# Kernel tuning notes

Measured on AMD Instinct MI355X. Metric: run time of the kernel, lower is better.

The kernel has to match this reference:

```python
import jax, jax.numpy as jnp
import numpy as np

# Dimensions
B, T, H = 4, 4096, 2048          # batch, seq, hidden
NH = 16                           # total hash heads = (max_ngram-1)*n_head_per_ngram
PER_HEAD_VOCAB = 100000
DH = 64                           # per-head embedding dim
E = NH * DH                       # engram_hidden_size = 1024
G = 4                             # hc_mult
K = 4                             # kernel_size
DIL = 3                           # dilation = max_ngram_size
EPS_RMS = 1.1920929e-07           # torch RMSNorm default eps (fp32 finfo eps)
EPS_SC = 1e-5                     # ShortConv RMSNorm eps


def setup_inputs() -> dict:
    key = jax.random.key(0)
    ks = jax.random.split(key, 12)
    hidden_states = jax.random.normal(ks[0], (T, B, H), dtype=jnp.float32)
    hash_ids = jax.random.randint(ks[1], (B, T, NH), 0, PER_HEAD_VOCAB)
    emb_table = jax.random.normal(ks[2], (NH * PER_HEAD_VOCAB, DH), dtype=jnp.float32)
    s = 0.02
    key_W = jax.random.normal(ks[3], (G, H, E), dtype=jnp.float32) * s
    key_b = jax.random.normal(ks[4], (G, H), dtype=jnp.float32) * s
    value_W = jax.random.normal(ks[5], (H, E), dtype=jnp.float32) * s
    value_b = jax.random.normal(ks[6], (H,), dtype=jnp.float32) * s
    norm1_w = jnp.ones((G, H), dtype=jnp.float32)
    norm2_w = jnp.ones((G, H), dtype=jnp.float32)
    sc_norm_w = jnp.ones((G, H), dtype=jnp.float32)
    conv_w = jax.random.normal(ks[7], (G * H, K), dtype=jnp.float32) * 0.1
    return {"hidden_states": hidden_states, "hash_ids": hash_ids, "emb_table": emb_table,
            "key_W": key_W, "key_b": key_b, "value_W": value_W, "value_b": value_b,
            "norm1_w": norm1_w, "norm2_w": norm2_w, "sc_norm_w": sc_norm_w, "conv_w": conv_w}


def _rms(x, eps):
    return x * jax.lax.rsqrt(jnp.mean(x * x, axis=-1, keepdims=True) + eps)


def reference(hidden_states, hash_ids, emb_table, key_W, key_b, value_W, value_b,
              norm1_w, norm2_w, sc_norm_w, conv_w):
    # --- precompute_embeddings: hashed multi-head gather ---
    offsets = jnp.arange(NH, dtype=hash_ids.dtype) * PER_HEAD_VOCAB
    emb = emb_table[hash_ids + offsets]              # [B,T,NH,DH]
    emb = emb.reshape(B, T, E)                       # [B,T,E]

    # --- forward ---
    hs = jnp.transpose(hidden_states, (1, 0, 2))     # [B,T,H]
    # per-group key projection + RMSNorm (vectorized over G)
    keys = jnp.einsum('bte,ghe->btgh', emb, key_W) + key_b   # [B,T,G,H]
    nk = _rms(keys, EPS_RMS) * norm1_w               # [B,T,G,H]
    nq = _rms(hs, EPS_RMS)[:, :, None, :] * norm2_w  # [B,T,G,H]
    gate = jnp.sum(nk * nq, axis=-1) / np.sqrt(H)    # [B,T,G]
    gate = jnp.sqrt(jnp.maximum(jnp.abs(gate), 1e-6)) * jnp.sign(gate)
    gate = jax.nn.sigmoid(gate)[..., None]           # [B,T,G,1]
    value = gate * (emb @ value_W.T + value_b)[:, :, None, :]   # [B,T,G,H]

    # --- ShortConv: per-group RMSNorm -> causal dilated depthwise conv -> SiLU ---
    xn = _rms(value, EPS_SC) * sc_norm_w             # [B,T,G,H]
    x_bct = xn.reshape(B, T, G * H).transpose(0, 2, 1)  # [B,G*H,T]
    y = jax.lax.conv_general_dilated(
        x_bct, conv_w[:, None, :],                   # rhs [C,1,K]
        window_strides=(1,), padding=[((K - 1) * DIL, 0)],
        rhs_dilation=(DIL,), dimension_numbers=('NCH', 'OIH', 'NCH'),
        feature_group_count=G * H)                   # [B,G*H,T]
    y = jax.nn.silu(y)
    y = y.transpose(0, 2, 1).reshape(B, T, G, H)

    out = (value + y).mean(axis=2)                   # [B,T,H]
    return jnp.transpose(out, (1, 0, 2))             # [S,B,H]
```

## Files before the change

kernel.cpp:

```cpp
#include <hip/hip_runtime.h>
#include <hip/hip_bf16.h>

#define BB 4
#define TT 4096
#define HH 2048
#define NHH 16
#define VOC 100000
#define EE 1024
#define GG 4
#define BT (BB*TT)
#define NKEY (GG*HH)
#define NTOT (NKEY+HH)
#define NPART 32
#define TCV 48

static constexpr float EPS_RMS = 1.1920929e-07f;
static constexpr float EPS_SC  = 1e-5f;
static constexpr float INV_SQRT_H = 0.02209708691207961f;

using f32x4 = __attribute__((ext_vector_type(4))) float;
using f32x2 = __attribute__((ext_vector_type(2))) float;
using s8v   = __attribute__((ext_vector_type(8))) short;
using gvoid = __attribute__((address_space(1))) const void;
using lvoid = __attribute__((address_space(3))) void;

__device__ __forceinline__ unsigned short f2bf(float f){
  union { __hip_bfloat16 h; unsigned short u; } cv;
  cv.h = __float2bfloat16(f);
  return cv.u;
}
__device__ __forceinline__ float bf2f(unsigned short u){
  union { float f; unsigned u; } cv;
  cv.u = ((unsigned)u) << 16;
  return cv.f;
}

__global__ __launch_bounds__(256) void convw_kern(const float* __restrict__ kW,
    const float* __restrict__ vW, unsigned short* __restrict__ Wc){
  const long idx  = (long)blockIdx.x*256 + threadIdx.x;
  const long base = idx*4;
  const long KN   = (long)NKEY*EE;
  float4 v;
  if (base < KN) v = *(const float4*)(kW + base);
  else           v = *(const float4*)(vW + (base - KN));
  ushort4 o; o.x=f2bf(v.x); o.y=f2bf(v.y); o.z=f2bf(v.z); o.w=f2bf(v.w);
  *(ushort4*)(Wc + base) = o;
}

__global__ __launch_bounds__(256) void prep_kern(const int* __restrict__ hids,
    const float* __restrict__ table, unsigned short* __restrict__ emb,
    const float* __restrict__ hs, float* __restrict__ rq,
    unsigned short* __restrict__ hsbf){
  const int p = blockIdx.x, tid = threadIdx.x;
  const int e = tid*4, head = e>>6, d = e&63;
  const long row = (long)hids[p*NHH + head] + (long)head*VOC;
  const float4 v = *(const float4*)(table + row*64 + d);
  ushort4 o; o.x=f2bf(v.x); o.y=f2bf(v.y); o.z=f2bf(v.z); o.w=f2bf(v.w);
  *(ushort4*)(emb + (size_t)p*EE + e) = o;
  const int b = p>>12, t = p&4095;
  const float* hrow = hs + ((size_t)t*BB + b)*HH;
  const int e8 = tid*8;
  float4 v0 = *(const float4*)(hrow+e8);
  float4 v1 = *(const float4*)(hrow+e8+4);
  ushort4 hb0; hb0.x=f2bf(v0.x); hb0.y=f2bf(v0.y); hb0.z=f2bf(v0.z); hb0.w=f2bf(v0.w);
  ushort4 hb1; hb1.x=f2bf(v1.x); hb1.y=f2bf(v1.y); hb1.z=f2bf(v1.z); hb1.w=f2bf(v1.w);
  *(ushort4*)(hsbf + (size_t)p*HH + e8)     = hb0;
  *(ushort4*)(hsbf + (size_t)p*HH + e8 + 4) = hb1;
  float s = v0.x*v0.x+v0.y*v0.y+v0.z*v0.z+v0.w*v0.w
          + v1.x*v1.x+v1.y*v1.y+v1.z*v1.z+v1.w*v1.w;
  #pragma unroll
  for (int of=32;of>=1;of>>=1) s += __shfl_xor(s,of);
  __shared__ float red[4];
  if ((tid&63)==0) red[tid>>6] = s;
  __syncthreads();
  if (tid==0){
    float tot = red[0]+red[1]+red[2]+red[3];
    rq[p] = rsqrtf(tot*(1.0f/HH) + EPS_RMS);
  }
}

__global__ __launch_bounds__(512, 2) void gemm8(
    const unsigned short* __restrict__ A, const unsigned short* __restrict__ Bw,
    const float* __restrict__ key_b, const float* __restrict__ value_b,
    const float* __restrict__ n1w, const float* __restrict__ n2w,
    const unsigned short* __restrict__ hsbf, unsigned short* __restrict__ vlinb,
    f32x2* __restrict__ sdp, float* __restrict__ vsqp)
{
  __shared__ unsigned short sh[65536];
  const int tid = threadIdx.x, w = tid>>6, l = tid&63;
  const int wm = w>>2, wn = w&3;
  const int lg = l&15, lr = l>>4;
  const int wg  = blockIdx.x;
  const int swz = (wg&7)*320 + (wg>>3);
  const int tM  = swz/40, tN = swz - tM*40;
  const int Mrow0 = tM*256, Nrow0 = tN*256;

  const int lp = l>>3, lcs = (l&7)^lp;
  const size_t aoffT = (size_t)(Mrow0 + w*16 + lp)*EE + lcs*8;
  const size_t boffT = (size_t)(Nrow0 + w*16 + lp)*EE + lcs*8;
  const int c0 = lr ^ (lg&7);
  const unsigned aBase = (unsigned)(wm*8192 + lg*64);
  const unsigned bBase = (unsigned)(16384 + (wn>>1)*8192 + (wn&1)*4096 + lg*64);

  f32x4 acc[8][4] = {};
  s8v aR0[4], aR1[4], bR0[4], bR1[4];

#define STAGEH(ISB, H, KT, SB) { \
    const unsigned short* s0_ = ((ISB) ? (Bw + boffT) : (A + aoffT)) + (H)*131072 + (KT)*64; \
    const unsigned d0_ = (SB)*32768 + (ISB)*16384 + (H)*8192 + w*1024; \
    __builtin_amdgcn_global_load_lds((gvoid*)s0_,        (lvoid*)(sh + d0_),       16, 0, 0); \
    __builtin_amdgcn_global_load_lds((gvoid*)(s0_+8192), (lvoid*)(sh + d0_ + 512), 16, 0, 0); \
  }
#define STAGE4(KT, SB) { STAGEH(0,0,KT,SB); STAGEH(0,1,KT,SB); STAGEH(1,0,KT,SB); STAGEH(1,1,KT,SB); }

#define BAR() { asm volatile("" ::: "memory"); __builtin_amdgcn_s_barrier(); asm volatile("" ::: "memory"); }

#define RD_A(CB, KK, MH, DST) { \
    const unsigned short* p_ = sh + (CB)*32768 + aBase; \
    const unsigned ck_ = (unsigned)((c0 ^ ((KK)<<2))<<3); \
    DST[0] = *(const s8v*)(p_ + ((MH)*4+0)*1024 + ck_); \
    DST[1] = *(const s8v*)(p_ + ((MH)*4+1)*1024 + ck_); \
    DST[2] = *(const s8v*)(p_ + ((MH)*4+2)*1024 + ck_); \
    DST[3] = *(const s8v*)(p_ + ((MH)*4+3)*1024 + ck_); }

#define RD_B(CB, KK, DST) { \
    const unsigned short* p_ = sh + (CB)*32768 + bBase; \
    const unsigned ck_ = (unsigned)((c0 ^ ((KK)<<2))<<3); \
    DST[0] = *(const s8v*)(p_ + 0*1024 + ck_); \
    DST[1] = *(const s8v*)(p_ + 1*1024 + ck_); \
    DST[2] = *(const s8v*)(p_ + 2*1024 + ck_); \
    DST[3] = *(const s8v*)(p_ + 3*1024 + ck_); }

#define MM(MH, AF, BF) { \
    __builtin_amdgcn_s_setprio(1); \
    _Pragma("unroll") \
    for (int mf=0; mf<4; mf++) \
      _Pragma("unroll") \
      for (int nf=0; nf<4; nf++) \
        acc[(MH)*4+mf][nf] = __builtin_amdgcn_mfma_f32_16x16x32_bf16(AF[mf], BF[nf], acc[(MH)*4+mf][nf], 0,0,0); \
    __builtin_amdgcn_s_setprio(0); }

#define TILE(CB, NB, KT1, DOST) { \
    BAR(); \
    if (DOST) STAGE4(KT1, NB); \
    RD_A(CB,1,0,aR1); RD_B(CB,1,bR1); \
    MM(0, aR0, bR0); \
    RD_A(CB,0,1,aR0); \
    MM(0, aR1, bR1); \
    RD_A(CB,1,1,aR1); \
    MM(1, aR0, bR0); \
    asm volatile("s_waitcnt vmcnt(0)" ::: "memory"); \
    BAR(); \
    RD_A(NB,0,0,aR0); RD_B(NB,0,bR0); \
    MM(1, aR1, bR1); }

#define TILE_LAST(CB) { \
    BAR(); \
    RD_A(CB,1,0,aR1); RD_B(CB,1,bR1); \
    MM(0, aR0, bR0); \
    RD_A(CB,0,1,aR0); \
    MM(0, aR1, bR1); \
    RD_A(CB,1,1,aR1); \
    MM(1, aR0, bR0); \
    MM(1, aR1, bR1); }

  STAGE4(0, 0);
  asm volatile("s_waitcnt vmcnt(0)" ::: "memory");
  BAR();
  RD_A(0,0,0,aR0); RD_B(0,0,bR0);

  #pragma unroll 1
  for (int i=0; i<7; i++){
    const int kt = 2*i;
    TILE(0, 1, kt+1, true);
    TILE(1, 0, kt+2, true);
  }
  TILE(0, 1, 15, true);
  TILE_LAST(1);

#undef STAGEH
#undef STAGE4
#undef RD_A
#undef RD_B
#undef MM
#undef TILE
#undef TILE_LAST

  BAR();

  const bool isK = (Nrow0 < NKEY);
  float bias[4], cw[4]; int hcol[4];
  #pragma unroll
  for (int nf=0; nf<4; nf++){
    const int n = Nrow0 + wn*64 + nf*16 + lg;
    hcol[nf] = n & (HH-1);
    if (isK){ bias[nf] = key_b[n]; cw[nf] = n1w[n]*n2w[n]; }
    else    { bias[nf] = value_b[n-NKEY]; cw[nf] = 0.f; }
  }

  if (isK){
    const int g = Nrow0 >> 11;
    const int slot = (tN&7)*4 + wn;
    char* wreg = (char*)sh + w*16384;
    #pragma unroll
    for (int mfa=0; mfa<8; mfa++){
      #pragma unroll
      for (int rr=0; rr<4; rr++){
        const int rowl = mfa*16 + lr*4 + rr;
        const int p = Mrow0 + wm*128 + rowl;
        const unsigned short* hrow = hsbf + (size_t)p*HH;
        float ssq=0.f, dt=0.f;
        #pragma unroll
        for (int nf=0; nf<4; nf++){
          const float c = acc[mfa][nf][rr] + bias[nf];
          ssq += c*c;
          dt  += c * cw[nf] * bf2f(hrow[hcol[nf]]);
        }
        f32x2 pr; pr[0]=ssq; pr[1]=dt;
        *(f32x2*)(wreg + rowl*128 + (((lg>>1) ^ (rowl&7))<<4) + ((lg&1)<<3)) = pr;
      }
    }
    #pragma unroll
    for (int rh=0; rh<2; rh++){
      const int r = l + rh*64;
      float ssq=0.f, dt=0.f;
      #pragma unroll
      for (int c=0; c<8; c++){
        f32x4 v = *(const f32x4*)(wreg + r*128 + ((c ^ (r&7))<<4));
        ssq += v[0] + v[2]; dt += v[1] + v[3];
      }
      const int p = Mrow0 + wm*128 + r;
      f32x2 o; o[0]=ssq; o[1]=dt;
      sdp[(size_t)(p*GG+g)*NPART + slot] = o;
    }
  } else {
    const int slot = (tN-32)*4 + wn;
    const int h0 = Nrow0 - NKEY + wn*64;
    const int pbase = Mrow0 + wm*128;
    #pragma unroll
    for (int mfa=0; mfa<8; mfa++){
      #pragma unroll
      for (int rr=0; rr<4; rr++){
        const int p = pbase + mfa*16 + lr*4 + rr;
        float ssq=0.f;
        #pragma unroll
        for (int nf=0; nf<4; nf++){
          const float c = acc[mfa][nf][rr] + bias[nf];
          vlinb[(size_t)p*HH + h0 + nf*16 + lg] = f2bf(c);
          ssq += c*c;
        }
        #pragma unroll
        for (int o=1;o<16;o<<=1){ ssq += __shfl_xor(ssq,o); }
        if (lg==0) vsqp[(size_t)p*NPART + slot] = ssq;
      }
    }
  }
}

__global__ __launch_bounds__(256) void scal_kern(const f32x2* __restrict__ sdp,
    const float* __restrict__ vsqp,
    const float* __restrict__ rq, float* __restrict__ gate, float* __restrict__ av){
  const int i = blockIdx.x*256 + threadIdx.x;
  const int p = i>>2;
  float ss=0.f, dd=0.f, vv=0.f;
  const f32x2* sp = sdp + (size_t)i*NPART;
  #pragma unroll
  for (int j=0;j<NPART;j++){ f32x2 v = sp[j]; ss += v[0]; dd += v[1]; }
  #pragma unroll
  for (int j=0;j<NPART;j++){ vv += vsqp[(size_t)p*NPART+j]; }
  const float rk = rsqrtf(ss*(1.0f/HH) + EPS_RMS);
  const float gv = rk * rq[p] * dd * INV_SQRT_H;
  const float sgn = (gv>0.f)?1.f:((gv<0.f)?-1.f:0.f);
  const float g1 = sqrtf(fmaxf(fabsf(gv),1e-6f))*sgn;
  const float gt = 1.f/(1.f+__expf(-g1));
  const float msvl = vv*(1.0f/HH);
  const float a = gt * rsqrtf(gt*gt*msvl + EPS_SC);
  gate[i]=gt; av[i]=a;
}

__device__ __forceinline__ ushort4 ldrow(const unsigned short* __restrict__ v, int b, int t, int h0){
  if (t < 0){ ushort4 z; z.x=0;z.y=0;z.z=0;z.w=0; return z; }
  return *(const ushort4*)(v + (size_t)((b<<12)|t)*HH + h0);
}
__device__ __forceinline__ void ldav(const float* __restrict__ av, int b, int t, float* a){
  if (t < 0){ a[0]=0.f;a[1]=0.f;a[2]=0.f;a[3]=0.f; }
  else { const float4 x = *(const float4*)(av + (size_t)((b<<12)|t)*GG);
         a[0]=x.x;a[1]=x.y;a[2]=x.z;a[3]=x.w; }
}

__global__ __launch_bounds__(256) void conv2_kern(const unsigned short* __restrict__ vlinb,
    const float* __restrict__ gate, const float* __restrict__ av,
    const float* __restrict__ conv_w, const float* __restrict__ scw,
    float* __restrict__ out){
  const int bx = blockIdx.x;
  const int b  = blockIdx.y;
  const int t0 = (bx>>1)*TCV;
  const int h0 = (bx&1)*1024 + threadIdx.x*4;

  float cwv[4][4][4];
  float sc4[4][4];
  #pragma unroll
  for (int g=0; g<4; g++){
    #pragma unroll
    for (int j2=0; j2<4; j2++){
      const int c = g*HH + h0 + j2;
      const float4 wv = *(const float4*)(conv_w + (size_t)c*4);
      cwv[g][j2][0]=wv.x; cwv[g][j2][1]=wv.y; cwv[g][j2][2]=wv.z; cwv[g][j2][3]=wv.w;
      sc4[g][j2] = scw[c];
    }
  }

  #pragma unroll 1
  for (int r=0; r<3; r++){
    const int tf = t0 + r;
    ushort4 w0 = ldrow(vlinb, b, tf-9, h0);
    ushort4 w1 = ldrow(vlinb, b, tf-6, h0);
    ushort4 w2 = ldrow(vlinb, b, tf-3, h0);
    ushort4 w3; w3.x=0;w3.y=0;w3.z=0;w3.w=0;
    #pragma unroll
    for (int j=0; j<16; j++){
      const int t = tf + 3*j;
      if (t < TT){
        const int p = (b<<12)|t;
        w3 = *(const ushort4*)(vlinb + (size_t)p*HH + h0);
        float a0[4],a1[4],a2[4],a3[4];
        ldav(av, b, t-9, a0); ldav(av, b, t-6, a1); ldav(av, b, t-3, a2); ldav(av, b, t, a3);
        float gt4[4];
        { const float4 x = *(const float4*)(gate + (size_t)p*GG);
          gt4[0]=x.x; gt4[1]=x.y; gt4[2]=x.z; gt4[3]=x.w; }
        float v0[4],v1[4],v2[4],v3[4];
        v0[0]=bf2f(w0.x); v0[1]=bf2f(w0.y); v0[2]=bf2f(w0.z); v0[3]=bf2f(w0.w);
        v1[0]=bf2f(w1.x); v1[1]=bf2f(w1.y); v1[2]=bf2f(w1.z); v1[3]=bf2f(w1.w);
        v2[0]=bf2f(w2.x); v2[1]=bf2f(w2.y); v2[2]=bf2f(w2.z); v2[3]=bf2f(w2.w);
        v3[0]=bf2f(w3.x); v3[1]=bf2f(w3.y); v3[2]=bf2f(w3.z); v3[3]=bf2f(w3.w);
        float4 ov;
        float res[4];
        #pragma unroll
        for (int j2=0; j2<4; j2++){
          float acc = 0.f;
          #pragma unroll
          for (int g=0; g<4; g++){
            float y = cwv[g][j2][0]*a0[g]*v0[j2]
                    + cwv[g][j2][1]*a1[g]*v1[j2]
                    + cwv[g][j2][2]*a2[g]*v2[j2]
                    + cwv[g][j2][3]*a3[g]*v3[j2];
            y *= sc4[g][j2];
            const float sy = y * (1.f/(1.f+__expf(-y)));
            acc += gt4[g]*v3[j2] + sy;
          }
          res[j2] = acc*0.25f;
        }
        ov.x=res[0]; ov.y=res[1]; ov.z=res[2]; ov.w=res[3];
        *(float4*)(out + ((size_t)t*BB + b)*HH + h0) = ov;
      }
      w0=w1; w1=w2; w2=w3;
    }
  }
}

extern "C" void kernel_launch(void* const* d_in, const int* in_sizes, int n_in,
                              void* d_out, int out_size, void* d_ws, size_t ws_size,
                              hipStream_t stream){
  (void)in_sizes; (void)n_in; (void)out_size; (void)ws_size;
  const float* hs    = (const float*)d_in[0];
  const int*   hids  = (const int*)d_in[1];
  const float* table = (const float*)d_in[2];
  const float* keyW  = (const float*)d_in[3];
  const float* keyB  = (const float*)d_in[4];
  const float* valW  = (const float*)d_in[5];
  const float* valB  = (const float*)d_in[6];
  const float* n1w   = (const float*)d_in[7];
  const float* n2w   = (const float*)d_in[8];
  const float* scw   = (const float*)d_in[9];
  const float* convw = (const float*)d_in[10];
  float* out = (float*)d_out;

  char* ws = (char*)d_ws;
  size_t off = 0;
  unsigned short* emb   = (unsigned short*)(ws+off); off += (size_t)BT*EE*2;
  unsigned short* Wc    = (unsigned short*)(ws+off); off += (size_t)NTOT*EE*2;
  unsigned short* vlinb = (unsigned short*)(ws+off); off += (size_t)BT*HH*2;
  unsigned short* hsbf  = (unsigned short*)(ws+off); off += (size_t)BT*HH*2;
  f32x2* sdp    = (f32x2*)(ws+off); off += (size_t)BT*GG*NPART*8;
  float* vsqp   = (float*)(ws+off); off += (size_t)BT*NPART*4;
  float* rq     = (float*)(ws+off); off += (size_t)BT*4;
  float* gate   = (float*)(ws+off); off += (size_t)BT*GG*4;
  float* av     = (float*)(ws+off); off += (size_t)BT*GG*4;

  convw_kern<<<(NTOT*EE/4)/256, 256, 0, stream>>>(keyW, valW, Wc);
  prep_kern<<<BT, 256, 0, stream>>>(hids, table, emb, hs, rq, hsbf);
  gemm8<<<2560, 512, 0, stream>>>(emb, Wc, keyB, valB, n1w, n2w, hsbf, vlinb, sdp, vsqp);
  scal_kern<<<(BT*GG)/256, 256, 0, stream>>>(sdp, vsqp, rq, gate, av);
  dim3 cg(((TT + TCV - 1)/TCV)*2, BB);
  conv2_kern<<<cg, 256, 0, stream>>>(vlinb, gate, av, convw, scw, out);
}
```

Before: 554.5 us.

## Pre-pack B weights into MFMA fragment layout and load directly to registers

The weight conversion kernel now writes B in a layout that matches the MFMA fragment order, so the GEMM loads B fragments straight from global memory into registers instead of staging them through LDS. This halves LDS use for the main loop and removes B LDS reads and barriers-related traffic, at the cost of uncoalesced-ish per-wave global loads that depend on L2 reuse and may expose latency. The key-branch epilogue now stages the needed hidden-state bf16 slice into LDS with coalesced loads instead of scattered per-element global reads. The conv kernel also reuses the av loads across iterations with a sliding window.

Result: slower. 616.0 us (+11.1%).

```diff
diff --git a/kernel.cpp b/kernel.cpp
--- a/kernel.cpp
+++ b/kernel.cpp
@@ -34,17 +34,27 @@
   cv.u = ((unsigned)u) << 16;
   return cv.f;
 }
-
-__global__ __launch_bounds__(256) void convw_kern(const float* __restrict__ kW,
-    const float* __restrict__ vW, unsigned short* __restrict__ Wc){
-  const long idx  = (long)blockIdx.x*256 + threadIdx.x;
-  const long base = idx*4;
-  const long KN   = (long)NKEY*EE;
-  float4 v;
-  if (base < KN) v = *(const float4*)(kW + base);
-  else           v = *(const float4*)(vW + (base - KN));
-  ushort4 o; o.x=f2bf(v.x); o.y=f2bf(v.y); o.z=f2bf(v.z); o.w=f2bf(v.w);
-  *(ushort4*)(Wc + base) = o;
+__device__ __forceinline__ s8v pack8(float4 v0, float4 v1){
+  s8v o;
+  o[0]=(short)f2bf(v0.x); o[1]=(short)f2bf(v0.y); o[2]=(short)f2bf(v0.z); o[3]=(short)f2bf(v0.w);
+  o[4]=(short)f2bf(v1.x); o[5]=(short)f2bf(v1.y); o[6]=(short)f2bf(v1.z); o[7]=(short)f2bf(v1.w);
+  return o;
+}
+
+__global__ __launch_bounds__(256) void convw_pack(const float* __restrict__ kW,
+    const float* __restrict__ vW, unsigned short* __restrict__ Bpk){
+  const int nb = blockIdx.x;
+  const int t = threadIdx.x, lane = t&63, q = t>>6;
+  const int n = nb*16 + (lane&15);
+  const float* src = (n < NKEY) ? (kW + (size_t)n*EE) : (vW + (size_t)(n-NKEY)*EE);
+  #pragma unroll
+  for (int i=0;i<8;i++){
+    const int kb = q*8 + i;
+    const int k0 = kb*32 + (lane>>4)*8;
+    float4 v0 = *(const float4*)(src + k0);
+    float4 v1 = *(const float4*)(src + k0 + 4);
+    *(s8v*)(Bpk + (size_t)(nb*32 + kb)*512 + lane*8) = pack8(v0, v1);
+  }
 }
 
 __global__ __launch_bounds__(256) void prep_kern(const int* __restrict__ hids,
@@ -62,10 +72,7 @@
   const int e8 = tid*8;
   float4 v0 = *(const float4*)(hrow+e8);
   float4 v1 = *(const float4*)(hrow+e8+4);
-  ushort4 hb0; hb0.x=f2bf(v0.x); hb0.y=f2bf(v0.y); hb0.z=f2bf(v0.z); hb0.w=f2bf(v0.w);
-  ushort4 hb1; hb1.x=f2bf(v1.x); hb1.y=f2bf(v1.y); hb1.z=f2bf(v1.z); hb1.w=f2bf(v1.w);
-  *(ushort4*)(hsbf + (size_t)p*HH + e8)     = hb0;
-  *(ushort4*)(hsbf + (size_t)p*HH + e8 + 4) = hb1;
+  *(s8v*)(hsbf + (size_t)p*HH + e8) = pack8(v0, v1);
   float s = v0.x*v0.x+v0.y*v0.y+v0.z*v0.z+v0.w*v0.w
           + v1.x*v1.x+v1.y*v1.y+v1.z*v1.z+v1.w*v1.w;
   #pragma unroll
@@ -80,7 +87,7 @@
 }
 
 __global__ __launch_bounds__(512, 2) void gemm8(
-    const unsigned short* __restrict__ A, const unsigned short* __restrict__ Bw,
+    const unsigned short* __restrict__ A, const unsigned short* __restrict__ Bpk,
     const float* __restrict__ key_b, const float* __restrict__ value_b,
     const float* __restrict__ n1w, const float* __restrict__ n2w,
     const unsigned short* __restrict__ hsbf, unsigned short* __restrict__ vlinb,
@@ -97,39 +104,40 @@
 
   const int lp = l>>3, lcs = (l&7)^lp;
   const size_t aoffT = (size_t)(Mrow0 + w*16 + lp)*EE + lcs*8;
-  const size_t boffT = (size_t)(Nrow0 + w*16 + lp)*EE + lcs*8;
   const int c0 = lr ^ (lg&7);
   const unsigned aBase = (unsigned)(wm*8192 + lg*64);
-  const unsigned bBase = (unsigned)(16384 + (wn>>1)*8192 + (wn&1)*4096 + lg*64);
+  const unsigned bof0 = (unsigned)(tN*16 + wn*4 + 0)*32u*512u + (unsigned)l*8u;
+  const unsigned bof1 = (unsigned)(tN*16 + wn*4 + 1)*32u*512u + (unsigned)l*8u;
+  const unsigned bof2 = (unsigned)(tN*16 + wn*4 + 2)*32u*512u + (unsigned)l*8u;
+  const unsigned bof3 = (unsigned)(tN*16 + wn*4 + 3)*32u*512u + (unsigned)l*8u;
 
   f32x4 acc[8][4] = {};
   s8v aR0[4], aR1[4], bR0[4], bR1[4];
 
-#define STAGEH(ISB, H, KT, SB) { \
-    const unsigned short* s0_ = ((ISB) ? (Bw + boffT) : (A + aoffT)) + (H)*131072 + (KT)*64; \
-    const unsigned d0_ = (SB)*32768 + (ISB)*16384 + (H)*8192 + w*1024; \
-    __builtin_amdgcn_global_load_lds((gvoid*)s0_,        (lvoid*)(sh + d0_),       16, 0, 0); \
-    __builtin_amdgcn_global_load_lds((gvoid*)(s0_+8192), (lvoid*)(sh + d0_ + 512), 16, 0, 0); \
-  }
-#define STAGE4(KT, SB) { STAGEH(0,0,KT,SB); STAGEH(0,1,KT,SB); STAGEH(1,0,KT,SB); STAGEH(1,1,KT,SB); }
-
 #define BAR() { asm volatile("" ::: "memory"); __builtin_amdgcn_s_barrier(); asm volatile("" ::: "memory"); }
+#define WAITV(N) asm volatile("s_waitcnt vmcnt(" #N ")" ::: "memory")
+
+#define STG_A(J, KT, SB) { \
+    const unsigned short* s_ = A + aoffT + (J)*131072 + (KT)*64; \
+    const unsigned d_ = (SB)*16384 + (J)*8192 + w*1024; \
+    __builtin_amdgcn_global_load_lds((gvoid*)s_,        (lvoid*)(sh + d_),       16, 0, 0); \
+    __builtin_amdgcn_global_load_lds((gvoid*)(s_+8192), (lvoid*)(sh + d_ + 512), 16, 0, 0); }
+#define STAGE_A(KT, SB) { STG_A(0,KT,SB); STG_A(1,KT,SB); }
 
 #define RD_A(CB, KK, MH, DST) { \
-    const unsigned short* p_ = sh + (CB)*32768 + aBase; \
+    const unsigned short* p_ = sh + (CB)*16384 + aBase; \
     const unsigned ck_ = (unsigned)((c0 ^ ((KK)<<2))<<3); \
     DST[0] = *(const s8v*)(p_ + ((MH)*4+0)*1024 + ck_); \
     DST[1] = *(const s8v*)(p_ + ((MH)*4+1)*1024 + ck_); \
     DST[2] = *(const s8v*)(p_ + ((MH)*4+2)*1024 + ck_); \
     DST[3] = *(const s8v*)(p_ + ((MH)*4+3)*1024 + ck_); }
 
-#define RD_B(CB, KK, DST) { \
-    const unsigned short* p_ = sh + (CB)*32768 + bBase; \
-    const unsigned ck_ = (unsigned)((c0 ^ ((KK)<<2))<<3); \
-    DST[0] = *(const s8v*)(p_ + 0*1024 + ck_); \
-    DST[1] = *(const s8v*)(p_ + 1*1024 + ck_); \
-    DST[2] = *(const s8v*)(p_ + 2*1024 + ck_); \
-    DST[3] = *(const s8v*)(p_ + 3*1024 + ck_); }
+#define GLB(KT, KK, DST) { \
+    const unsigned short* q_ = Bpk + (unsigned)((KT)*2+(KK))*512u; \
+    DST[0] = *(const s8v*)(q_ + bof0); \
+    DST[1] = *(const s8v*)(q_ + bof1); \
+    DST[2] = *(const s8v*)(q_ + bof2); \
+    DST[3] = *(const s8v*)(q_ + bof3); }
 
 #define MM(MH, AF, BF) { \
     __builtin_amdgcn_s_setprio(1); \
@@ -140,23 +148,26 @@
         acc[(MH)*4+mf][nf] = __builtin_amdgcn_mfma_f32_16x16x32_bf16(AF[mf], BF[nf], acc[(MH)*4+mf][nf], 0,0,0); \
     __builtin_amdgcn_s_setprio(0); }
 
-#define TILE(CB, NB, KT1, DOST) { \
+#define TILE(CB, NB, KT0, KT1, DOST) { \
     BAR(); \
-    if (DOST) STAGE4(KT1, NB); \
-    RD_A(CB,1,0,aR1); RD_B(CB,1,bR1); \
+    if (DOST) STAGE_A(KT1, NB); \
+    GLB(KT0, 1, bR1); \
+    RD_A(CB,1,0,aR1); \
     MM(0, aR0, bR0); \
     RD_A(CB,0,1,aR0); \
     MM(0, aR1, bR1); \
     RD_A(CB,1,1,aR1); \
     MM(1, aR0, bR0); \
-    asm volatile("s_waitcnt vmcnt(0)" ::: "memory"); \
+    WAITV(0); \
     BAR(); \
-    RD_A(NB,0,0,aR0); RD_B(NB,0,bR0); \
+    GLB(KT1, 0, bR0); \
+    RD_A(NB,0,0,aR0); \
     MM(1, aR1, bR1); }
 
-#define TILE_LAST(CB) { \
+#define TILE_LAST(CB, KT0) { \
     BAR(); \
-    RD_A(CB,1,0,aR1); RD_B(CB,1,bR1); \
+    GLB(KT0, 1, bR1); \
+    RD_A(CB,1,0,aR1); \
     MM(0, aR0, bR0); \
     RD_A(CB,0,1,aR0); \
     MM(0, aR1, bR1); \
@@ -164,74 +175,96 @@
     MM(1, aR0, bR0); \
     MM(1, aR1, bR1); }
 
-  STAGE4(0, 0);
-  asm volatile("s_waitcnt vmcnt(0)" ::: "memory");
+  STAGE_A(0, 0);
+  STAGE_A(1, 1);
+  GLB(0, 0, bR0);
+  WAITV(0);
   BAR();
-  RD_A(0,0,0,aR0); RD_B(0,0,bR0);
+  RD_A(0,0,0,aR0);
 
   #pragma unroll 1
   for (int i=0; i<7; i++){
-    const int kt = 2*i;
-    TILE(0, 1, kt+1, true);
-    TILE(1, 0, kt+2, true);
-  }
-  TILE(0, 1, 15, true);
-  TILE_LAST(1);
-
-#undef STAGEH
-#undef STAGE4
+    TILE(0, 1, 2*i,   2*i+1, true);
+    TILE(1, 0, 2*i+1, 2*i+2, true);
+  }
+  TILE(0, 1, 14, 15, true);
+  TILE_LAST(1, 15);
+
+#undef STG_A
+#undef STAGE_A
 #undef RD_A
-#undef RD_B
+#undef GLB
 #undef MM
 #undef TILE
 #undef TILE_LAST
-
-  BAR();
+#undef BAR
+#undef WAITV
+
+  __syncthreads();
 
   const bool isK = (Nrow0 < NKEY);
-  float bias[4], cw[4]; int hcol[4];
+  float bias[4], cw[4];
   #pragma unroll
   for (int nf=0; nf<4; nf++){
     const int n = Nrow0 + wn*64 + nf*16 + lg;
-    hcol[nf] = n & (HH-1);
     if (isK){ bias[nf] = key_b[n]; cw[nf] = n1w[n]*n2w[n]; }
     else    { bias[nf] = value_b[n-NKEY]; cw[nf] = 0.f; }
   }
 
   if (isK){
-    const int g = Nrow0 >> 11;
+    const int g = tN >> 3;
     const int slot = (tN&7)*4 + wn;
-    char* wreg = (char*)sh + w*16384;
+    const int colbase = (tN&7)*256;
+    unsigned short* hsT = sh;
+    char* wreg = ((char*)sh) + 65536 + w*8192;
     #pragma unroll
-    for (int mfa=0; mfa<8; mfa++){
+    for (int half=0; half<2; half++){
       #pragma unroll
-      for (int rr=0; rr<4; rr++){
-        const int rowl = mfa*16 + lr*4 + rr;
-        const int p = Mrow0 + wm*128 + rowl;
-        const unsigned short* hrow = hsbf + (size_t)p*HH;
-        float ssq=0.f, dt=0.f;
+      for (int pass=0; pass<8; pass++){
+        const int r2 = pass*16 + (tid>>5);
+        const int c8 = (tid&31)*8;
+        const int p = Mrow0 + half*128 + r2;
+        s8v wv = *(const s8v*)(hsbf + (size_t)p*HH + colbase + c8);
+        *(s8v*)(hsT + r2*256 + (c8 ^ (((r2>>2)&3)<<4))) = wv;
+      }
+      __syncthreads();
+      if (wm == half){
         #pragma unroll
-        for (int nf=0; nf<4; nf++){
-          const float c = acc[mfa][nf][rr] + bias[nf];
-          ssq += c*c;
-          dt  += c * cw[nf] * bf2f(hrow[hcol[nf]]);
+        for (int pass2=0; pass2<2; pass2++){
+          #pragma unroll
+          for (int mfs=0; mfs<4; mfs++){
+            const int mfa = pass2*4 + mfs;
+            #pragma unroll
+            for (int rr=0; rr<4; rr++){
+              const int rowq = mfs*16 + lr*4 + rr;
+              const int rowlh = pass2*64 + rowq;
+              float ssq=0.f, dt=0.f;
+              #pragma unroll
+              for (int nf=0; nf<4; nf++){
+                const float c = acc[mfa][nf][rr] + bias[nf];
+                const float hv = bf2f(hsT[rowlh*256 + wn*64 + ((nf^lr)<<4) + lg]);
+                ssq += c*c;
+                dt  += c * cw[nf] * hv;
+              }
+              f32x2 pr; pr[0]=ssq; pr[1]=dt;
+              *(f32x2*)(wreg + rowq*128 + (((lg>>1) ^ (rowq&7))<<4) + ((lg&1)<<3)) = pr;
+            }
+          }
+          {
+            const int r = l;
+            float ssq=0.f, dt=0.f;
+            #pragma unroll
+            for (int c=0; c<8; c++){
+              f32x4 v = *(const f32x4*)(wreg + r*128 + ((c ^ (r&7))<<4));
+              ssq += v[0] + v[2]; dt += v[1] + v[3];
+            }
+            const int p = Mrow0 + wm*128 + pass2*64 + r;
+            f32x2 o2; o2[0]=ssq; o2[1]=dt;
+            sdp[(size_t)(p*GG+g)*NPART + slot] = o2;
+          }
         }
-        f32x2 pr; pr[0]=ssq; pr[1]=dt;
-        *(f32x2*)(wreg + rowl*128 + (((lg>>1) ^ (rowl&7))<<4) + ((lg&1)<<3)) = pr;
       }
-    }
-    #pragma unroll
-    for (int rh=0; rh<2; rh++){
-      const int r = l + rh*64;
-      float ssq=0.f, dt=0.f;
-      #pragma unroll
-      for (int c=0; c<8; c++){
-        f32x4 v = *(const f32x4*)(wreg + r*128 + ((c ^ (r&7))<<4));
-        ssq += v[0] + v[2]; dt += v[1] + v[3];
-      }
-      const int p = Mrow0 + wm*128 + r;
-      f32x2 o; o[0]=ssq; o[1]=dt;
-      sdp[(size_t)(p*GG+g)*NPART + slot] = o;
+      __syncthreads();
     }
   } else {
     const int slot = (tN-32)*4 + wn;
@@ -317,17 +350,18 @@
     ushort4 w1 = ldrow(vlinb, b, tf-6, h0);
     ushort4 w2 = ldrow(vlinb, b, tf-3, h0);
     ushort4 w3; w3.x=0;w3.y=0;w3.z=0;w3.w=0;
+    float a0[4],a1[4],a2[4],a3[4];
+    ldav(av, b, tf-9, a0); ldav(av, b, tf-6, a1); ldav(av, b, tf-3, a2);
     #pragma unroll
     for (int j=0; j<16; j++){
       const int t = tf + 3*j;
       if (t < TT){
         const int p = (b<<12)|t;
         w3 = *(const ushort4*)(vlinb + (size_t)p*HH + h0);
-        float a0[4],a1[4],a2[4],a3[4];
-        ldav(av, b, t-9, a0); ldav(av, b, t-6, a1); ldav(av, b, t-3, a2); ldav(av, b, t, a3);
+        ldav(av, b, t, a3);
         float gt4[4];
-        { const float4 x = *(const float4*)(gate + (size_t)p*GG);
-          gt4[0]=x.x; gt4[1]=x.y; gt4[2]=x.z; gt4[3]=x.w; }
+        { const float4 xx = *(const float4*)(gate + (size_t)p*GG);
+          gt4[0]=xx.x; gt4[1]=xx.y; gt4[2]=xx.z; gt4[3]=xx.w; }
         float v0[4],v1[4],v2[4],v3[4];
         v0[0]=bf2f(w0.x); v0[1]=bf2f(w0.y); v0[2]=bf2f(w0.z); v0[3]=bf2f(w0.w);
         v1[0]=bf2f(w1.x); v1[1]=bf2f(w1.y); v1[2]=bf2f(w1.z); v1[3]=bf2f(w1.w);
@@ -354,6 +388,8 @@
         *(float4*)(out + ((size_t)t*BB + b)*HH + h0) = ov;
       }
       w0=w1; w1=w2; w2=w3;
+      #pragma unroll
+      for (int g=0; g<4; g++){ a0[g]=a1[g]; a1[g]=a2[g]; a2[g]=a3[g]; }
     }
   }
 }
@@ -378,7 +414,7 @@
   char* ws = (char*)d_ws;
   size_t off = 0;
   unsigned short* emb   = (unsigned short*)(ws+off); off += (size_t)BT*EE*2;
-  unsigned short* Wc    = (unsigned short*)(ws+off); off += (size_t)NTOT*EE*2;
+  unsigned short* Bpk   = (unsigned short*)(ws+off); off += (size_t)NTOT*EE*2;
   unsigned short* vlinb = (unsigned short*)(ws+off); off += (size_t)BT*HH*2;
   unsigned short* hsbf  = (unsigned short*)(ws+off); off += (size_t)BT*HH*2;
   f32x2* sdp    = (f32x2*)(ws+off); off += (size_t)BT*GG*NPART*8;
@@ -387,9 +423,9 @@
   float* gate   = (float*)(ws+off); off += (size_t)BT*GG*4;
   float* av     = (float*)(ws+off); off += (size_t)BT*GG*4;
 
-  convw_kern<<<(NTOT*EE/4)/256, 256, 0, stream>>>(keyW, valW, Wc);
+  convw_pack<<<NTOT/16, 256, 0, stream>>>(keyW, valW, Bpk);
   prep_kern<<<BT, 256, 0, stream>>>(hids, table, emb, hs, rq, hsbf);
-  gemm8<<<2560, 512, 0, stream>>>(emb, Wc, keyB, valB, n1w, n2w, hsbf, vlinb, sdp, vsqp);
+  gemm8<<<2560, 512, 0, stream>>>(emb, Bpk, keyB, valB, n1w, n2w, hsbf, vlinb, sdp, vsqp);
   scal_kern<<<(BT*GG)/256, 256, 0, stream>>>(sdp, vsqp, rq, gate, av);
   dim3 cg(((TT + TCV - 1)/TCV)*2, BB);
   conv2_kern<<<cg, 256, 0, stream>>>(vlinb, gate, av, convw, scw, out);
```

## Restructure GEMM main loop into quadrant phases with finer LDS pipelining

Applied to the files above, without the earlier changes.

Splits each K-tile of the fused key/value GEMM into four quadrant phases. Each phase stages one slice of the next tile and issues partial vmcnt/lgkmcnt waits, so global-to-LDS loads overlap MFMA work at finer grain. Each wave now owns a 2x2 set of 64x32 quadrants instead of a 128x64 block. The key epilogue first stages hidden-state bf16 rows into LDS with a swizzle rather than reading them from global per lane. Smaller edits pack the bf16 hidden store into one 16-byte write and keep a sliding window of the av loads in the conv kernel. More barriers and a more complex schedule risk sync overhead and occupancy changes.

Result: faster. 542.3 us (-2.2%).

```diff
diff --git a/kernel.cpp b/kernel.cpp
--- a/kernel.cpp
+++ b/kernel.cpp
@@ -33,6 +33,12 @@
   union { float f; unsigned u; } cv;
   cv.u = ((unsigned)u) << 16;
   return cv.f;
+}
+__device__ __forceinline__ s8v pack8(float4 v0, float4 v1){
+  s8v o;
+  o[0]=(short)f2bf(v0.x); o[1]=(short)f2bf(v0.y); o[2]=(short)f2bf(v0.z); o[3]=(short)f2bf(v0.w);
+  o[4]=(short)f2bf(v1.x); o[5]=(short)f2bf(v1.y); o[6]=(short)f2bf(v1.z); o[7]=(short)f2bf(v1.w);
+  return o;
 }
 
 __global__ __launch_bounds__(256) void convw_kern(const float* __restrict__ kW,
@@ -62,10 +68,7 @@
   const int e8 = tid*8;
   float4 v0 = *(const float4*)(hrow+e8);
   float4 v1 = *(const float4*)(hrow+e8+4);
-  ushort4 hb0; hb0.x=f2bf(v0.x); hb0.y=f2bf(v0.y); hb0.z=f2bf(v0.z); hb0.w=f2bf(v0.w);
-  ushort4 hb1; hb1.x=f2bf(v1.x); hb1.y=f2bf(v1.y); hb1.z=f2bf(v1.z); hb1.w=f2bf(v1.w);
-  *(ushort4*)(hsbf + (size_t)p*HH + e8)     = hb0;
-  *(ushort4*)(hsbf + (size_t)p*HH + e8 + 4) = hb1;
+  *(s8v*)(hsbf + (size_t)p*HH + e8) = pack8(v0, v1);
   float s = v0.x*v0.x+v0.y*v0.y+v0.z*v0.z+v0.w*v0.w
           + v1.x*v1.x+v1.y*v1.y+v1.z*v1.z+v1.w*v1.w;
   #pragma unroll
@@ -88,7 +91,7 @@
 {
   __shared__ unsigned short sh[65536];
   const int tid = threadIdx.x, w = tid>>6, l = tid&63;
-  const int wm = w>>2, wn = w&3;
+  const int wr = w>>2, wc = w&3;
   const int lg = l&15, lr = l>>4;
   const int wg  = blockIdx.x;
   const int swz = (wg&7)*320 + (wg>>3);
@@ -99,11 +102,16 @@
   const size_t aoffT = (size_t)(Mrow0 + w*16 + lp)*EE + lcs*8;
   const size_t boffT = (size_t)(Nrow0 + w*16 + lp)*EE + lcs*8;
   const int c0 = lr ^ (lg&7);
-  const unsigned aBase = (unsigned)(wm*8192 + lg*64);
-  const unsigned bBase = (unsigned)(16384 + (wn>>1)*8192 + (wn&1)*4096 + lg*64);
-
-  f32x4 acc[8][4] = {};
-  s8v aR0[4], aR1[4], bR0[4], bR1[4];
+  const unsigned ck0 = (unsigned)(c0<<3);
+  const unsigned ck1 = (unsigned)((c0^4)<<3);
+  const unsigned aBase = (unsigned)(wr*4096 + lg*64);
+  const unsigned bBase = 16384u + (unsigned)(wc*2048 + lg*64);
+
+  f32x4 acc[4][4][2] = {};
+  s8v aK0[4], aK1[4];
+  s8v b0[2][2], b1[2][2];
+
+#define BAR() { asm volatile("" ::: "memory"); __builtin_amdgcn_s_barrier(); asm volatile("" ::: "memory"); }
 
 #define STAGEH(ISB, H, KT, SB) { \
     const unsigned short* s0_ = ((ISB) ? (Bw + boffT) : (A + aoffT)) + (H)*131072 + (KT)*64; \
@@ -111,147 +119,196 @@
     __builtin_amdgcn_global_load_lds((gvoid*)s0_,        (lvoid*)(sh + d0_),       16, 0, 0); \
     __builtin_amdgcn_global_load_lds((gvoid*)(s0_+8192), (lvoid*)(sh + d0_ + 512), 16, 0, 0); \
   }
-#define STAGE4(KT, SB) { STAGEH(0,0,KT,SB); STAGEH(0,1,KT,SB); STAGEH(1,0,KT,SB); STAGEH(1,1,KT,SB); }
-
-#define BAR() { asm volatile("" ::: "memory"); __builtin_amdgcn_s_barrier(); asm volatile("" ::: "memory"); }
-
-#define RD_A(CB, KK, MH, DST) { \
-    const unsigned short* p_ = sh + (CB)*32768 + aBase; \
-    const unsigned ck_ = (unsigned)((c0 ^ ((KK)<<2))<<3); \
-    DST[0] = *(const s8v*)(p_ + ((MH)*4+0)*1024 + ck_); \
-    DST[1] = *(const s8v*)(p_ + ((MH)*4+1)*1024 + ck_); \
-    DST[2] = *(const s8v*)(p_ + ((MH)*4+2)*1024 + ck_); \
-    DST[3] = *(const s8v*)(p_ + ((MH)*4+3)*1024 + ck_); }
-
-#define RD_B(CB, KK, DST) { \
-    const unsigned short* p_ = sh + (CB)*32768 + bBase; \
-    const unsigned ck_ = (unsigned)((c0 ^ ((KK)<<2))<<3); \
-    DST[0] = *(const s8v*)(p_ + 0*1024 + ck_); \
-    DST[1] = *(const s8v*)(p_ + 1*1024 + ck_); \
-    DST[2] = *(const s8v*)(p_ + 2*1024 + ck_); \
-    DST[3] = *(const s8v*)(p_ + 3*1024 + ck_); }
-
-#define MM(MH, AF, BF) { \
+
+#define RD_AQ(CB, QR) { \
+    const unsigned short* p_ = sh + (CB)*32768 + (QR)*8192 + aBase; \
+    aK0[0]=*(const s8v*)(p_+0*1024+ck0); aK0[1]=*(const s8v*)(p_+1*1024+ck0); \
+    aK0[2]=*(const s8v*)(p_+2*1024+ck0); aK0[3]=*(const s8v*)(p_+3*1024+ck0); \
+    aK1[0]=*(const s8v*)(p_+0*1024+ck1); aK1[1]=*(const s8v*)(p_+1*1024+ck1); \
+    aK1[2]=*(const s8v*)(p_+2*1024+ck1); aK1[3]=*(const s8v*)(p_+3*1024+ck1); }
+
+#define RD_BQ(CB, QC, B) { \
+    const unsigned short* p_ = sh + (CB)*32768 + (QC)*8192 + bBase; \
+    B[0][0]=*(const s8v*)(p_+0*1024+ck0); B[0][1]=*(const s8v*)(p_+1*1024+ck0); \
+    B[1][0]=*(const s8v*)(p_+0*1024+ck1); B[1][1]=*(const s8v*)(p_+1*1024+ck1); }
+
+#define MMQ(QR, QC, B) { \
     __builtin_amdgcn_s_setprio(1); \
     _Pragma("unroll") \
-    for (int mf=0; mf<4; mf++) \
-      _Pragma("unroll") \
-      for (int nf=0; nf<4; nf++) \
-        acc[(MH)*4+mf][nf] = __builtin_amdgcn_mfma_f32_16x16x32_bf16(AF[mf], BF[nf], acc[(MH)*4+mf][nf], 0,0,0); \
+    for (int mf=0; mf<4; mf++){ \
+      acc[(QR)*2+(QC)][mf][0] = __builtin_amdgcn_mfma_f32_16x16x32_bf16(aK0[mf], B[0][0], acc[(QR)*2+(QC)][mf][0], 0,0,0); \
+      acc[(QR)*2+(QC)][mf][1] = __builtin_amdgcn_mfma_f32_16x16x32_bf16(aK0[mf], B[0][1], acc[(QR)*2+(QC)][mf][1], 0,0,0); \
+    } \
+    _Pragma("unroll") \
+    for (int mf=0; mf<4; mf++){ \
+      acc[(QR)*2+(QC)][mf][0] = __builtin_amdgcn_mfma_f32_16x16x32_bf16(aK1[mf], B[1][0], acc[(QR)*2+(QC)][mf][0], 0,0,0); \
+      acc[(QR)*2+(QC)][mf][1] = __builtin_amdgcn_mfma_f32_16x16x32_bf16(aK1[mf], B[1][1], acc[(QR)*2+(QC)][mf][1], 0,0,0); \
+    } \
     __builtin_amdgcn_s_setprio(0); }
 
-#define TILE(CB, NB, KT1, DOST) { \
+#define LGKM0() { asm volatile("s_waitcnt lgkmcnt(0)" ::: "memory"); __builtin_amdgcn_sched_barrier(0); }
+
+#define PH0(CB, NB, KT1, DOST, VM) { \
+    RD_AQ(CB, 0); RD_BQ(CB, 0, b0); \
+    if (DOST) STAGEH(0,0,KT1,NB); \
+    asm volatile("s_waitcnt lgkmcnt(8)" ::: "memory"); \
+    BAR(); LGKM0(); \
+    MMQ(0,0,b0); \
+    VM; BAR(); }
+
+#define PH1(CB, NB, KT1, DOST, VM) { \
+    RD_BQ(CB, 1, b1); \
+    if (DOST) STAGEH(1,0,KT1,NB); \
+    BAR(); LGKM0(); \
+    MMQ(0,1,b1); \
+    VM; BAR(); }
+
+#define PH2(CB, NB, KT1, DOST) { \
+    RD_AQ(CB, 1); \
+    if (DOST) STAGEH(1,1,KT1,NB); \
+    BAR(); LGKM0(); \
+    MMQ(1,0,b0); \
+    BAR(); }
+
+#define PH3(CB, NB, KT1, DOST, VM) { \
+    if (DOST) STAGEH(0,1,KT1,NB); \
     BAR(); \
-    if (DOST) STAGE4(KT1, NB); \
-    RD_A(CB,1,0,aR1); RD_B(CB,1,bR1); \
-    MM(0, aR0, bR0); \
-    RD_A(CB,0,1,aR0); \
-    MM(0, aR1, bR1); \
-    RD_A(CB,1,1,aR1); \
-    MM(1, aR0, bR0); \
-    asm volatile("s_waitcnt vmcnt(0)" ::: "memory"); \
-    BAR(); \
-    RD_A(NB,0,0,aR0); RD_B(NB,0,bR0); \
-    MM(1, aR1, bR1); }
-
-#define TILE_LAST(CB) { \
-    BAR(); \
-    RD_A(CB,1,0,aR1); RD_B(CB,1,bR1); \
-    MM(0, aR0, bR0); \
-    RD_A(CB,0,1,aR0); \
-    MM(0, aR1, bR1); \
-    RD_A(CB,1,1,aR1); \
-    MM(1, aR0, bR0); \
-    MM(1, aR1, bR1); }
-
-  STAGE4(0, 0);
-  asm volatile("s_waitcnt vmcnt(0)" ::: "memory");
+    MMQ(1,1,b1); \
+    VM; BAR(); }
+
+#define VM4 asm volatile("s_waitcnt vmcnt(4)" ::: "memory")
+#define VM2 asm volatile("s_waitcnt vmcnt(2)" ::: "memory")
+#define VM0 asm volatile("s_waitcnt vmcnt(0)" ::: "memory")
+#define VMN (void)0
+
+#define TILE_STD(CB, NB, KT1) { \
+    PH0(CB, NB, KT1, 1, VM4); \
+    PH1(CB, NB, KT1, 1, VM4); \
+    PH2(CB, NB, KT1, 1); \
+    PH3(CB, NB, KT1, 1, VM4); }
+
+  STAGEH(0,0,0,0); STAGEH(1,0,0,0); STAGEH(1,1,0,0); STAGEH(0,1,0,0);
+  VM4;
   BAR();
-  RD_A(0,0,0,aR0); RD_B(0,0,bR0);
 
   #pragma unroll 1
   for (int i=0; i<7; i++){
-    const int kt = 2*i;
-    TILE(0, 1, kt+1, true);
-    TILE(1, 0, kt+2, true);
-  }
-  TILE(0, 1, 15, true);
-  TILE_LAST(1);
-
+    TILE_STD(0, 1, 2*i+1);
+    TILE_STD(1, 0, 2*i+2);
+  }
+  TILE_STD(0, 1, 15);
+  PH0(1, 0, 0, 0, VM2);
+  PH1(1, 0, 0, 0, VM0);
+  PH2(1, 0, 0, 0);
+  PH3(1, 0, 0, 0, VMN);
+
+#undef BAR
 #undef STAGEH
-#undef STAGE4
-#undef RD_A
-#undef RD_B
-#undef MM
-#undef TILE
-#undef TILE_LAST
-
-  BAR();
+#undef RD_AQ
+#undef RD_BQ
+#undef MMQ
+#undef LGKM0
+#undef PH0
+#undef PH1
+#undef PH2
+#undef PH3
+#undef VM4
+#undef VM2
+#undef VM0
+#undef VMN
+#undef TILE_STD
+
+  __syncthreads();
 
   const bool isK = (Nrow0 < NKEY);
-  float bias[4], cw[4]; int hcol[4];
+  float bias[2][2], cw[2][2]; int ncol[2][2];
   #pragma unroll
-  for (int nf=0; nf<4; nf++){
-    const int n = Nrow0 + wn*64 + nf*16 + lg;
-    hcol[nf] = n & (HH-1);
-    if (isK){ bias[nf] = key_b[n]; cw[nf] = n1w[n]*n2w[n]; }
-    else    { bias[nf] = value_b[n-NKEY]; cw[nf] = 0.f; }
+  for (int QC=0; QC<2; QC++){
+    #pragma unroll
+    for (int nf=0; nf<2; nf++){
+      const int n = Nrow0 + QC*128 + wc*32 + nf*16 + lg;
+      ncol[QC][nf] = QC*128 + wc*32 + nf*16 + lg;
+      if (isK){ bias[QC][nf] = key_b[n]; cw[QC][nf] = n1w[n]*n2w[n]; }
+      else    { bias[QC][nf] = value_b[n-NKEY]; cw[QC][nf] = 0.f; }
+    }
   }
 
   if (isK){
-    const int g = Nrow0 >> 11;
-    const int slot = (tN&7)*4 + wn;
-    char* wreg = (char*)sh + w*16384;
+    const int g = tN >> 3;
+    const int slot = (tN&7)*4 + wc;
+    const int colbase = (tN&7)*256;
+    unsigned short* hsT = sh;
+    char* wreg = ((char*)sh) + 65536 + w*8192;
     #pragma unroll
-    for (int mfa=0; mfa<8; mfa++){
+    for (int QR=0; QR<2; QR++){
       #pragma unroll
-      for (int rr=0; rr<4; rr++){
-        const int rowl = mfa*16 + lr*4 + rr;
-        const int p = Mrow0 + wm*128 + rowl;
-        const unsigned short* hrow = hsbf + (size_t)p*HH;
+      for (int pass=0; pass<8; pass++){
+        const int r2 = pass*16 + (tid>>5);
+        const int c8 = (tid&31)*8;
+        const int p = Mrow0 + QR*128 + r2;
+        s8v wv = *(const s8v*)(hsbf + (size_t)p*HH + colbase + c8);
+        *(s8v*)(hsT + r2*256 + (c8 ^ (((r2>>2)&3)<<4))) = wv;
+      }
+      __syncthreads();
+      #pragma unroll
+      for (int mf=0; mf<4; mf++){
+        #pragma unroll
+        for (int rr=0; rr<4; rr++){
+          const int rowq = mf*16 + lr*4 + rr;
+          const int rowh = wr*64 + rowq;
+          float ssq=0.f, dt=0.f;
+          #pragma unroll
+          for (int QC=0; QC<2; QC++){
+            #pragma unroll
+            for (int nf=0; nf<2; nf++){
+              const float c = acc[QR*2+QC][mf][nf][rr] + bias[QC][nf];
+              const float hv = bf2f(hsT[rowh*256 + (ncol[QC][nf] ^ (lr<<4))]);
+              ssq += c*c;
+              dt  += c * cw[QC][nf] * hv;
+            }
+          }
+          f32x2 pr; pr[0]=ssq; pr[1]=dt;
+          *(f32x2*)(wreg + rowq*128 + (((lg>>1) ^ (rowq&7))<<4) + ((lg&1)<<3)) = pr;
+        }
+      }
+      {
+        const int r = l;
         float ssq=0.f, dt=0.f;
         #pragma unroll
-        for (int nf=0; nf<4; nf++){
-          const float c = acc[mfa][nf][rr] + bias[nf];
-          ssq += c*c;
-          dt  += c * cw[nf] * bf2f(hrow[hcol[nf]]);
+        for (int c=0; c<8; c++){
+          f32x4 v = *(const f32x4*)(wreg + r*128 + ((c ^ (r&7))<<4));
+          ssq += v[0] + v[2]; dt += v[1] + v[3];
         }
-        f32x2 pr; pr[0]=ssq; pr[1]=dt;
-        *(f32x2*)(wreg + rowl*128 + (((lg>>1) ^ (rowl&7))<<4) + ((lg&1)<<3)) = pr;
+        const int p = Mrow0 + QR*128 + wr*64 + r;
+        f32x2 o2; o2[0]=ssq; o2[1]=dt;
+        sdp[(size_t)(p*GG+g)*NPART + slot] = o2;
       }
-    }
-    #pragma unroll
-    for (int rh=0; rh<2; rh++){
-      const int r = l + rh*64;
-      float ssq=0.f, dt=0.f;
-      #pragma unroll
-      for (int c=0; c<8; c++){
-        f32x4 v = *(const f32x4*)(wreg + r*128 + ((c ^ (r&7))<<4));
-        ssq += v[0] + v[2]; dt += v[1] + v[3];
-      }
-      const int p = Mrow0 + wm*128 + r;
-      f32x2 o; o[0]=ssq; o[1]=dt;
-      sdp[(size_t)(p*GG+g)*NPART + slot] = o;
+      __syncthreads();
     }
   } else {
-    const int slot = (tN-32)*4 + wn;
-    const int h0 = Nrow0 - NKEY + wn*64;
-    const int pbase = Mrow0 + wm*128;
+    const int slot = (tN-32)*4 + wc;
+    const int hbase = Nrow0 - NKEY;
     #pragma unroll
-    for (int mfa=0; mfa<8; mfa++){
+    for (int QR=0; QR<2; QR++){
       #pragma unroll
-      for (int rr=0; rr<4; rr++){
-        const int p = pbase + mfa*16 + lr*4 + rr;
-        float ssq=0.f;
+      for (int mf=0; mf<4; mf++){
         #pragma unroll
-        for (int nf=0; nf<4; nf++){
-          const float c = acc[mfa][nf][rr] + bias[nf];
-          vlinb[(size_t)p*HH + h0 + nf*16 + lg] = f2bf(c);
-          ssq += c*c;
+        for (int rr=0; rr<4; rr++){
+          const int p = Mrow0 + QR*128 + wr*64 + mf*16 + lr*4 + rr;
+          float ssq=0.f;
+          #pragma unroll
+          for (int QC=0; QC<2; QC++){
+            #pragma unroll
+            for (int nf=0; nf<2; nf++){
+              const float c = acc[QR*2+QC][mf][nf][rr] + bias[QC][nf];
+              vlinb[(size_t)p*HH + hbase + ncol[QC][nf]] = f2bf(c);
+              ssq += c*c;
+            }
+          }
+          #pragma unroll
+          for (int o=1;o<16;o<<=1){ ssq += __shfl_xor(ssq,o); }
+          if (lg==0) vsqp[(size_t)p*NPART + slot] = ssq;
         }
-        #pragma unroll
-        for (int o=1;o<16;o<<=1){ ssq += __shfl_xor(ssq,o); }
-        if (lg==0) vsqp[(size_t)p*NPART + slot] = ssq;
       }
     }
   }
@@ -317,17 +374,18 @@
     ushort4 w1 = ldrow(vlinb, b, tf-6, h0);
     ushort4 w2 = ldrow(vlinb, b, tf-3, h0);
     ushort4 w3; w3.x=0;w3.y=0;w3.z=0;w3.w=0;
+    float a0[4],a1[4],a2[4],a3[4];
+    ldav(av, b, tf-9, a0); ldav(av, b, tf-6, a1); ldav(av, b, tf-3, a2);
     #pragma unroll
     for (int j=0; j<16; j++){
       const int t = tf + 3*j;
       if (t < TT){
         const int p = (b<<12)|t;
         w3 = *(const ushort4*)(vlinb + (size_t)p*HH + h0);
-        float a0[4],a1[4],a2[4],a3[4];
-        ldav(av, b, t-9, a0); ldav(av, b, t-6, a1); ldav(av, b, t-3, a2); ldav(av, b, t, a3);
+        ldav(av, b, t, a3);
         float gt4[4];
-        { const float4 x = *(const float4*)(gate + (size_t)p*GG);
-          gt4[0]=x.x; gt4[1]=x.y; gt4[2]=x.z; gt4[3]=x.w; }
+        { const float4 xx = *(const float4*)(gate + (size_t)p*GG);
+          gt4[0]=xx.x; gt4[1]=xx.y; gt4[2]=xx.z; gt4[3]=xx.w; }
         float v0[4],v1[4],v2[4],v3[4];
         v0[0]=bf2f(w0.x); v0[1]=bf2f(w0.y); v0[2]=bf2f(w0.z); v0[3]=bf2f(w0.w);
         v1[0]=bf2f(w1.x); v1[1]=bf2f(w1.y); v1[2]=bf2f(w1.z); v1[3]=bf2f(w1.w);
@@ -354,6 +412,8 @@
         *(float4*)(out + ((size_t)t*BB + b)*HH + h0) = ov;
       }
       w0=w1; w1=w2; w2=w3;
+      #pragma unroll
+      for (int g=0; g<4; g++){ a0[g]=a1[g]; a1[g]=a2[g]; a2[g]=a3[g]; }
     }
   }
 }
```
